# Kernel optimization log

Measured on AMD Instinct MI355X. Metric: run time of the kernel, lower is better.

Reference implementation:

```python
import jax, jax.numpy as jnp
import numpy as np

B, N, D, H = 2, 2048, 1024, 16
DK = D // H


def setup_inputs() -> dict:
    key = jax.random.key(0)
    ks = jax.random.split(key, 12)
    s = D ** -0.5
    inp = {
        "query": jax.random.normal(ks[0], (B, N, D), jnp.float32),
        "key": jax.random.normal(ks[1], (B, N, D), jnp.float32),
        "value": jax.random.normal(ks[2], (B, N, D), jnp.float32),
        # causal mask: 1 = keep, 0 = masked (matches create_causal_mask)
        "mask": jnp.tril(jnp.ones((N, N), jnp.int32)),
        "Wq": jax.random.normal(ks[3], (D, D), jnp.float32) * s,
        "bq": jnp.zeros((D,), jnp.float32),
        "Wk": jax.random.normal(ks[4], (D, D), jnp.float32) * s,
        "bk": jnp.zeros((D,), jnp.float32),
        "Wv": jax.random.normal(ks[5], (D, D), jnp.float32) * s,
        "bv": jnp.zeros((D,), jnp.float32),
        "Wo": jax.random.normal(ks[6], (D, D), jnp.float32) * s,
        "bo": jnp.zeros((D,), jnp.float32),
    }
    return inp


def reference(query, key, value, mask, Wq, bq, Wk, bk, Wv, bv, Wo, bo):
    scale = DK ** -0.5
    # Linear projections (torch nn.Linear: x @ W.T + b), split into heads -> [B,H,N,DK]
    q = (query @ Wq.T + bq).reshape(B, N, H, DK).transpose(0, 2, 1, 3)
    k = (key @ Wk.T + bk).reshape(B, N, H, DK).transpose(0, 2, 1, 3)
    v = (value @ Wv.T + bv).reshape(B, N, H, DK).transpose(0, 2, 1, 3)
    scores = jnp.einsum("bhqd,bhkd->bhqk", q, k) * scale  # [B,H,N,N]
    scores = jnp.where(mask[None, None, :, :] == 0, jnp.float32(-1e9), scores)
    attn = jax.nn.softmax(scores, axis=-1)
    ctx = jnp.einsum("bhqk,bhkd->bhqd", attn, v)  # [B,H,N,DK]
    ctx = ctx.transpose(0, 2, 1, 3).reshape(B, N, D)
    return ctx @ Wo.T + bo
```

## Files before the change

### kernel.cpp

```cpp
#include <hip/hip_runtime.h>
#include <hip/hip_bf16.h>

typedef __attribute__((ext_vector_type(4))) float f32x4;
typedef __attribute__((ext_vector_type(8))) __bf16 bf16x8;
typedef __attribute__((ext_vector_type(8))) unsigned short u16x8;
typedef __attribute__((ext_vector_type(4))) unsigned short u16x4;
typedef __attribute__((ext_vector_type(2))) unsigned int u32x2;
typedef unsigned short u16;

#define DEV static __device__ __forceinline__

DEV u16 f2bf(float f){
  unsigned u = __builtin_bit_cast(unsigned, f);
  u += 0x7fff + ((u >> 16) & 1);
  return (u16)(u >> 16);
}

DEV unsigned cvtpk(float lo, float hi){
  unsigned r;
  asm("v_cvt_pk_bf16_f32 %0, %1, %2" : "=v"(r) : "v"(lo), "v"(hi));
  return r;
}

DEV f32x4 mfma16(bf16x8 a, bf16x8 b, f32x4 c){
  return __builtin_amdgcn_mfma_f32_16x16x32_bf16(a, b, c, 0, 0, 0);
}

DEV void gload16(const void* g, void* l){
  __builtin_amdgcn_global_load_lds((const __attribute__((address_space(1))) void*)g,
                                   (__attribute__((address_space(3))) void*)l,
                                   16, 0, 0);
}

DEV float fexp2(float x){
#if __has_builtin(__builtin_amdgcn_exp2f)
  return __builtin_amdgcn_exp2f(x);
#else
  float r; asm("v_exp_f32 %0, %1" : "=v"(r) : "v"(x)); return r;
#endif
}

#define SCL 0.18033688011f
#define THR 11.0f
#define PLD 72

__global__ __launch_bounds__(256) void cvtW_k(
    const float* __restrict__ s0, const float* __restrict__ s1,
    const float* __restrict__ s2, const float* __restrict__ s3,
    u16* __restrict__ d0, u16* __restrict__ d1,
    u16* __restrict__ d2, u16* __restrict__ d3){
  const int y = blockIdx.y;
  const float* __restrict__ s = y==0?s0:y==1?s1:y==2?s2:s3;
  u16* __restrict__ d         = y==0?d0:y==1?d1:y==2?d2:d3;
  const int i = blockIdx.x*256 + threadIdx.x;
  f32x4 a = *(const f32x4*)&s[(size_t)i*8];
  f32x4 b = *(const f32x4*)&s[(size_t)i*8 + 4];
  u16x8 h;
  #pragma unroll
  for (int j = 0; j < 4; ++j){ h[j] = f2bf(a[j]); h[j+4] = f2bf(b[j]); }
  *(u16x8*)&d[(size_t)i*8] = h;
}

DEV bf16x8 rdH(const u16* Hs, int r, int kc, int lhi, int l7){
  int gr = (kc*4 + lhi) ^ l7;
  return *(const bf16x8*)&Hs[r*64 + gr*8];
}

DEV bf16x8 rdF(const float* Fs, int r, int kc, int lhi, int l15){
  int g0 = kc*8 + lhi*2, g1 = g0 + 1;
  f32x4 a = *(const f32x4*)&Fs[r*64 + ((g0 ^ l15)*4)];
  f32x4 b = *(const f32x4*)&Fs[r*64 + ((g1 ^ l15)*4)];
  union { unsigned u[4]; bf16x8 v; } x;
  x.u[0] = cvtpk(a[0], a[1]);
  x.u[1] = cvtpk(a[2], a[3]);
  x.u[2] = cvtpk(b[0], b[1]);
  x.u[3] = cvtpk(b[2], b[3]);
  return x.v;
}

__global__ __launch_bounds__(256) void gemm_qkv2(
    const float* __restrict__ Xq, const float* __restrict__ Xk, const float* __restrict__ Xv,
    const u16* __restrict__ Wq, const u16* __restrict__ Wk, const u16* __restrict__ Wv,
    const float* __restrict__ Bq, const float* __restrict__ Bk, const float* __restrict__ Bv,
    u16* __restrict__ Oq, u16* __restrict__ Ok, u16* __restrict__ Ov){
  __shared__ float Fs[128*64];
  __shared__ u16  Hs[128*64];

  const int f = blockIdx.x;
  const int xc = f & 7, g = f >> 3;
  const int p  = xc*12 + (g >> 3);
  const int bn8 = g & 7;
  const int z = p >> 5, bm32 = p & 31;
  const bool vt = (z == 2);
  const int bm = vt ? bn8 : bm32;
  const int bn = vt ? bm32 : bn8;

  const float* __restrict__ Xz = z==0 ? Xq : z==1 ? Xk : Xv;
  const u16*  __restrict__ Wz  = z==0 ? Wq : z==1 ? Wk : Wv;
  const float* __restrict__ bias = z==0 ? Bq : z==1 ? Bk : Bv;
  u16* __restrict__ C = z==0 ? Oq : z==1 ? Ok : Ov;
  const float qs = (z==0) ? SCL : 1.0f;

  const int tid = threadIdx.x, lane = tid & 63, w = tid >> 6;
  const int wr = w >> 1, wc = w & 1;
  const int l16 = lane & 15, lhi = lane >> 4, l7 = l16 & 7;

  const int frow = tid >> 4, fcol = ((tid & 15) ^ (frow & 15)) * 4;
  const int hrow = tid >> 3, hcol = ((tid & 7) ^ (hrow & 7)) * 8;
  const int fblk = vt ? bn : bm;
  const int hblk = vt ? bm : bn;
  const float* Fsrc = Xz + (size_t)(fblk*128 + frow)*1024 + fcol;
  const u16*  Hsrc  = Wz + (size_t)(hblk*128 + hrow)*1024 + hcol;

  f32x4 acc[4][4] = {};

  for (int k0 = 0; k0 < 1024; k0 += 64){
    __syncthreads();
    #pragma unroll
    for (int j = 0; j < 8; ++j)
      gload16(Fsrc + k0 + (size_t)j*16*1024, Fs + j*1024 + w*256);
    #pragma unroll
    for (int j = 0; j < 4; ++j)
      gload16(Hsrc + k0 + (size_t)j*32*1024, Hs + j*2048 + w*512);
    __syncthreads();

    #pragma unroll
    for (int kc = 0; kc < 2; ++kc){
      bf16x8 fa[4], fb[4];
      if (!vt){
        #pragma unroll
        for (int mi = 0; mi < 4; ++mi) fa[mi] = rdF(Fs, wr*64 + mi*16 + l16, kc, lhi, l16);
        #pragma unroll
        for (int nf = 0; nf < 4; ++nf) fb[nf] = rdH(Hs, wc*64 + nf*16 + l16, kc, lhi, l7);
      } else {
        #pragma unroll
        for (int mi = 0; mi < 4; ++mi) fa[mi] = rdH(Hs, wr*64 + mi*16 + l16, kc, lhi, l7);
        #pragma unroll
        for (int nf = 0; nf < 4; ++nf) fb[nf] = rdF(Fs, wc*64 + nf*16 + l16, kc, lhi, l16);
      }
      #pragma unroll
      for (int mi = 0; mi < 4; ++mi)
        #pragma unroll
        for (int nf = 0; nf < 4; ++nf)
          acc[mi][nf] = mfma16(fa[mi], fb[nf], acc[mi][nf]);
    }
  }

  #pragma unroll
  for (int mi = 0; mi < 4; ++mi){
    #pragma unroll
    for (int nf = 0; nf < 4; ++nf){
      int row0 = bm*128 + wr*64 + mi*16 + lhi*4;
      int col  = bn*128 + wc*64 + nf*16 + l16;
      float bc = bias[col];
      #pragma unroll
      for (int r = 0; r < 4; ++r){
        int row = row0 + r;
        float val = (acc[mi][nf][r] + (vt ? bias[row] : bc)) * qs;
        if (!vt){
          int b = row >> 11, n = row & 2047;
          int h = col >> 6,  dk = col & 63;
          C[(((size_t)(b*16 + h))*2048 + n)*64 + dk] = f2bf(val);
        } else {
          int h = row >> 6,  dk = row & 63;
          int b = col >> 11, n = col & 2047;
          C[(((size_t)(b*16 + h))*64 + dk)*2048 + n] = f2bf(val);
        }
      }
    }
  }
}

__global__ __launch_bounds__(256) void gemm_o64(const u16* __restrict__ A,
                                                const u16* __restrict__ Bw,
                                                const float* __restrict__ bias,
                                                float* __restrict__ C){
  __shared__ u16 As[64*32];
  __shared__ u16 Bs[128*32];
  const int f = blockIdx.x;
  const int bm = (f & 7)*8 + ((f >> 3) >> 3);
  const int bn = (f >> 3) & 7;
  const int tid  = threadIdx.x;
  const int lane = tid & 63, w = tid >> 6;
  const int wr = w >> 1, wc = w & 1;
  const int l16 = lane & 15, lhi = lane >> 4;

  const int srow = w*16 + (lane >> 2);
  const int scol = (lane & 3)*8;
  const u16* Asrc = A  + (size_t)(bm*64  + srow)*1024 + scol;
  const u16* Bsrc = Bw + (size_t)(bn*128 + srow)*1024 + scol;
  u16* Adst0 = As + w*512;
  u16* Bdst0 = Bs + w*512;

  f32x4 acc[2][4] = {};

  for (int k0 = 0; k0 < 1024; k0 += 32){
    __syncthreads();
    gload16(Asrc + k0,             Adst0);
    gload16(Bsrc + k0,             Bdst0);
    gload16(Bsrc + 64*1024 + k0,   Bdst0 + 2048);
    __syncthreads();

    bf16x8 af[2], bfr[4];
    #pragma unroll
    for (int mi = 0; mi < 2; ++mi)
      af[mi] = *(const bf16x8*)&As[(wr*32 + mi*16 + l16)*32 + lhi*8];
    #pragma unroll
    for (int nf = 0; nf < 4; ++nf)
      bfr[nf] = *(const bf16x8*)&Bs[(wc*64 + nf*16 + l16)*32 + lhi*8];
    #pragma unroll
    for (int mi = 0; mi < 2; ++mi)
      #pragma unroll
      for (int nf = 0; nf < 4; ++nf)
        acc[mi][nf] = mfma16(af[mi], bfr[nf], acc[mi][nf]);
  }

  #pragma unroll
  for (int mi = 0; mi < 2; ++mi){
    #pragma unroll
    for (int nf = 0; nf < 4; ++nf){
      int row0 = bm*64 + wr*32 + mi*16 + lhi*4;
      int col  = bn*128 + wc*64 + nf*16 + l16;
      float bv = bias[col];
      #pragma unroll
      for (int r = 0; r < 4; ++r)
        C[(size_t)(row0 + r)*1024 + col] = acc[mi][nf][r] + bv;
    }
  }
}

DEV void sm_tile(int t, int qt, int q_abs,
                 const u16* __restrict__ Ksb, u16* __restrict__ PsW,
                 bf16x8 bq0, bf16x8 bq1,
                 f32x4* ctx, float& m_r, float& l_r,
                 int l16, int lhi, int lane, int swz){
  f32x4 s4[4] = {};
  #pragma unroll
  for (int nf = 0; nf < 4; ++nf){
    bf16x8 ak0 = *(const bf16x8*)&Ksb[(nf*16 + l16)*64 + ((lhi*8) ^ swz)];
    bf16x8 ak1 = *(const bf16x8*)&Ksb[(nf*16 + l16)*64 + ((32 + lhi*8) ^ swz)];
    s4[nf] = mfma16(ak0, bq0, s4[nf]);
    s4[nf] = mfma16(ak1, bq1, s4[nf]);
  }

  if (t == qt){
    #pragma unroll
    for (int nf = 0; nf < 4; ++nf)
      #pragma unroll
      for (int r = 0; r < 4; ++r){
        int kc = t*64 + nf*16 + lhi*4 + r;
        if (kc > q_abs) s4[nf][r] = -1.0e30f;
      }
  }

  float mt = fmaxf(
      fmaxf(fmaxf(fmaxf(s4[0][0],s4[0][1]), fmaxf(s4[0][2],s4[0][3])),
            fmaxf(fmaxf(s4[1][0],s4[1][1]), fmaxf(s4[1][2],s4[1][3]))),
      fmaxf(fmaxf(fmaxf(s4[2][0],s4[2][1]), fmaxf(s4[2][2],s4[2][3])),
            fmaxf(fmaxf(s4[3][0],s4[3][1]), fmaxf(s4[3][2],s4[3][3]))));
  mt = fmaxf(mt, __shfl_xor(mt, 16));
  mt = fmaxf(mt, __shfl_xor(mt, 32));

  if (!__all(mt <= m_r + THR)){
    float mn = fmaxf(m_r, mt);
    float sf = fexp2(m_r - mn);
    m_r = mn;
    l_r *= sf;
    float sfb[4];
    #pragma unroll
    for (int r = 0; r < 4; ++r)
      sfb[r] = __shfl(sf, (lane >> 4)*4 + r);
    #pragma unroll
    for (int dkf = 0; dkf < 4; ++dkf)
      #pragma unroll
      for (int r = 0; r < 4; ++r)
        ctx[dkf][r] *= sfb[r];
  }

  float lt = 0.f;
  u16* prow = PsW + l16*PLD;
  #pragma unroll
  for (int nf = 0; nf < 4; ++nf){
    float p0 = fexp2(s4[nf][0] - m_r);
    float p1 = fexp2(s4[nf][1] - m_r);
    float p2 = fexp2(s4[nf][2] - m_r);
    float p3 = fexp2(s4[nf][3] - m_r);
    lt += (p0 + p1) + (p2 + p3);
    unsigned w0 = __builtin_amdgcn_perm(__builtin_bit_cast(unsigned, p1),
                                        __builtin_bit_cast(unsigned, p0), 0x07060302u);
    unsigned w1 = __builtin_amdgcn_perm(__builtin_bit_cast(unsigned, p3),
                                        __builtin_bit_cast(unsigned, p2), 0x07060302u);
    u32x2 wp = {w0, w1};
    *(u32x2*)&prow[nf*16 + lhi*4] = wp;
  }
  lt += __shfl_xor(lt, 16);
  lt += __shfl_xor(lt, 32);
  l_r += lt;
}

DEV void pv_tile(const u16* __restrict__ Vsb, const u16* __restrict__ PsW,
                 f32x4* ctx, int l16, int lhi, int swz){
  const u16* prow = PsW + l16*PLD;
  __builtin_amdgcn_s_setprio(1);
  #pragma unroll
  for (int ks = 0; ks < 2; ++ks){
    bf16x8 pa = *(const bf16x8*)&prow[ks*32 + lhi*8];
    #pragma unroll
    for (int dkf = 0; dkf < 4; ++dkf){
      bf16x8 vb = *(const bf16x8*)&Vsb[(dkf*16 + l16)*64 + ((ks*32 + lhi*8) ^ swz)];
      ctx[dkf] = mfma16(pa, vb, ctx[dkf]);
    }
  }
  __builtin_amdgcn_s_setprio(0);
}

__global__ __launch_bounds__(256) void attn_k(const u16* __restrict__ Q,
                                              const u16* __restrict__ K,
                                              const u16* __restrict__ Vt,
                                              u16* __restrict__ CTX){
  __shared__ u16 Ks[2][64*64];
  __shared__ u16 Vs[2][64*64];
  __shared__ u16 Ps[4][2][16*PLD];
  const int tid  = threadIdx.x;
  const int lane = tid & 63, w = tid >> 6;
  const int l16 = lane & 15, lhi = lane >> 4;
  const int f  = blockIdx.x;
  const int bh = f & 31;
  const int qt = 31 - (f >> 5);
  const size_t base = (size_t)bh * 2048 * 64;
  const u16* Qb = Q  + base;
  const u16* Kb = K  + base;
  const u16* Vb = Vt + base;
  const int b = bh >> 4, h = bh & 15;

  const int s0 = tid, s1 = tid + 256;
  const int r0 = s0 >> 3, c0 = ((s0 & 7) ^ (r0 & 7))*8;
  const int r1 = s1 >> 3, c1 = ((s1 & 7) ^ (r1 & 7))*8;
  const u16* Ksrc0 = Kb + r0*64 + c0;
  const u16* Ksrc1 = Kb + r1*64 + c1;
  const u16* Vsrc0 = Vb + (size_t)r0*2048 + c0;
  const u16* Vsrc1 = Vb + (size_t)r1*2048 + c1;
  const int swz = (l16 & 7)*8;

  const int q_abs = qt*64 + w*16 + l16;
  bf16x8 bq0 = *(const bf16x8*)&Qb[(size_t)q_abs*64 + lhi*8];
  bf16x8 bq1 = *(const bf16x8*)&Qb[(size_t)q_abs*64 + 32 + lhi*8];

  f32x4 ctx[4] = {};
  float m_r = -3.0e38f, l_r = 0.f;
  u16* Ps0 = &Ps[w][0][0];
  u16* Ps1 = &Ps[w][1][0];

  gload16(Ksrc0, &Ks[0][s0*8]);  gload16(Ksrc1, &Ks[0][s1*8]);
  gload16(Vsrc0, &Vs[0][s0*8]);  gload16(Vsrc1, &Vs[0][s1*8]);
  __syncthreads();

  const int nt = qt + 1;
  for (int t = 0; t < nt; ++t){
    const int pb = t & 1;
    u16* PsC = pb ? Ps1 : Ps0;
    u16* PsP = pb ? Ps0 : Ps1;
    if (t + 1 < nt){
      gload16(Ksrc0 + (t+1)*4096, &Ks[pb^1][s0*8]);
      gload16(Ksrc1 + (t+1)*4096, &Ks[pb^1][s1*8]);
    }
    sm_tile(t, qt, q_abs, Ks[pb], PsC, bq0, bq1, ctx, m_r, l_r, l16, lhi, lane, swz);
    if (t > 0)
      pv_tile(Vs[pb^1], PsP, ctx, l16, lhi, swz);
    __syncthreads();
    if (t + 1 < nt){
      gload16(Vsrc0 + (size_t)(t+1)*64, &Vs[pb^1][s0*8]);
      gload16(Vsrc1 + (size_t)(t+1)*64, &Vs[pb^1][s1*8]);
    }
  }
  pv_tile(Vs[(nt-1)&1], (nt-1)&1 ? Ps1 : Ps0, ctx, l16, lhi, swz);

  float lf[4];
  #pragma unroll
  for (int r = 0; r < 4; ++r)
    lf[r] = __shfl(l_r, (lane >> 4)*4 + r);
  #pragma unroll
  for (int dkf = 0; dkf < 4; ++dkf)
    #pragma unroll
    for (int r = 0; r < 4; ++r){
      int q = qt*64 + w*16 + lhi*4 + r;
      CTX[((size_t)(b*2048 + q))*1024 + h*64 + dkf*16 + l16] = f2bf(ctx[dkf][r] / lf[r]);
    }
}

extern "C" void kernel_launch(void* const* d_in, const int* in_sizes, int n_in,
                              void* d_out, int out_size, void* d_ws, size_t ws_size,
                              hipStream_t stream){
  const float* q  = (const float*)d_in[0];
  const float* k  = (const float*)d_in[1];
  const float* v  = (const float*)d_in[2];
  const float* Wq = (const float*)d_in[4];  const float* bq = (const float*)d_in[5];
  const float* Wk = (const float*)d_in[6];  const float* bk = (const float*)d_in[7];
  const float* Wv = (const float*)d_in[8];  const float* bv = (const float*)d_in[9];
  const float* Wo = (const float*)d_in[10]; const float* bo = (const float*)d_in[11];
  float* out = (float*)d_out;
  dim3 blk(256);

  u16* Wqb = (u16*)d_ws;
  u16* Wkb = Wqb + 1048576;
  u16* Wvb = Wkb + 1048576;
  u16* Wob = Wvb + 1048576;
  u16* Qw  = Wob + 1048576;
  u16* Kw  = Qw + 4194304;
  u16* Vw  = Kw + 4194304;
  u16* Cw  = Vw + 4194304;

  cvtW_k<<<dim3(512, 4), blk, 0, stream>>>(Wq, Wk, Wv, Wo, Wqb, Wkb, Wvb, Wob);
  gemm_qkv2<<<dim3(768), blk, 0, stream>>>(q, k, v, Wqb, Wkb, Wvb,
                                           bq, bk, bv, Qw, Kw, Vw);
  attn_k<<<dim3(1024), blk, 0, stream>>>(Qw, Kw, Vw, Cw);
  gemm_o64<<<dim3(512), blk, 0, stream>>>(Cw, Wob, bo, out);
}
```

Baseline: 135.3 us.

## Pre-convert activations to bf16 in a separate pass and simplify QKV GEMM

```diff
diff --git a/kernel.cpp b/kernel.cpp
--- a/kernel.cpp
+++ b/kernel.cpp
@@ -16,12 +16,6 @@
   return (u16)(u >> 16);
 }
 
-DEV unsigned cvtpk(float lo, float hi){
-  unsigned r;
-  asm("v_cvt_pk_bf16_f32 %0, %1, %2" : "=v"(r) : "v"(lo), "v"(hi));
-  return r;
-}
-
 DEV f32x4 mfma16(bf16x8 a, bf16x8 b, f32x4 c){
   return __builtin_amdgcn_mfma_f32_16x16x32_bf16(a, b, c, 0, 0, 0);
 }
@@ -44,47 +38,40 @@
 #define THR 11.0f
 #define PLD 72
 
-__global__ __launch_bounds__(256) void cvtW_k(
+__global__ __launch_bounds__(256) void cvt_k(
     const float* __restrict__ s0, const float* __restrict__ s1,
     const float* __restrict__ s2, const float* __restrict__ s3,
-    u16* __restrict__ d0, u16* __restrict__ d1,
-    u16* __restrict__ d2, u16* __restrict__ d3){
+    const float* __restrict__ s4, const float* __restrict__ s5,
+    const float* __restrict__ s6,
+    u16* __restrict__ d0, u16* __restrict__ d1, u16* __restrict__ d2,
+    u16* __restrict__ d3, u16* __restrict__ d4, u16* __restrict__ d5,
+    u16* __restrict__ d6){
   const int y = blockIdx.y;
-  const float* __restrict__ s = y==0?s0:y==1?s1:y==2?s2:s3;
-  u16* __restrict__ d         = y==0?d0:y==1?d1:y==2?d2:d3;
-  const int i = blockIdx.x*256 + threadIdx.x;
-  f32x4 a = *(const f32x4*)&s[(size_t)i*8];
-  f32x4 b = *(const f32x4*)&s[(size_t)i*8 + 4];
-  u16x8 h;
-  #pragma unroll
-  for (int j = 0; j < 4; ++j){ h[j] = f2bf(a[j]); h[j+4] = f2bf(b[j]); }
-  *(u16x8*)&d[(size_t)i*8] = h;
-}
-
-DEV bf16x8 rdH(const u16* Hs, int r, int kc, int lhi, int l7){
-  int gr = (kc*4 + lhi) ^ l7;
-  return *(const bf16x8*)&Hs[r*64 + gr*8];
-}
-
-DEV bf16x8 rdF(const float* Fs, int r, int kc, int lhi, int l15){
-  int g0 = kc*8 + lhi*2, g1 = g0 + 1;
-  f32x4 a = *(const f32x4*)&Fs[r*64 + ((g0 ^ l15)*4)];
-  f32x4 b = *(const f32x4*)&Fs[r*64 + ((g1 ^ l15)*4)];
-  union { unsigned u[4]; bf16x8 v; } x;
-  x.u[0] = cvtpk(a[0], a[1]);
-  x.u[1] = cvtpk(a[2], a[3]);
-  x.u[2] = cvtpk(b[0], b[1]);
-  x.u[3] = cvtpk(b[2], b[3]);
-  return x.v;
-}
-
-__global__ __launch_bounds__(256) void gemm_qkv2(
-    const float* __restrict__ Xq, const float* __restrict__ Xk, const float* __restrict__ Xv,
+  const float* __restrict__ s = y==0?s0:y==1?s1:y==2?s2:y==3?s3:y==4?s4:y==5?s5:s6;
+  u16* __restrict__ d         = y==0?d0:y==1?d1:y==2?d2:y==3?d3:y==4?d4:y==5?d5:d6;
+  const int n8 = (y < 3) ? (4096*1024/8) : (1024*1024/8);
+  for (int i = blockIdx.x*256 + threadIdx.x; i < n8; i += gridDim.x*256){
+    f32x4 a = *(const f32x4*)&s[(size_t)i*8];
+    f32x4 b = *(const f32x4*)&s[(size_t)i*8 + 4];
+    u16x8 h;
+    #pragma unroll
+    for (int j = 0; j < 4; ++j){ h[j] = f2bf(a[j]); h[j+4] = f2bf(b[j]); }
+    *(u16x8*)&d[(size_t)i*8] = h;
+  }
+}
+
+DEV bf16x8 rdS(const u16* T, int r, int kc, int lhi){
+  int gr = (kc*4 + lhi) ^ (r & 7);
+  return *(const bf16x8*)&T[r*64 + gr*8];
+}
+
+__global__ __launch_bounds__(256) void gemm_qkv3(
+    const u16* __restrict__ Xq, const u16* __restrict__ Xk, const u16* __restrict__ Xv,
     const u16* __restrict__ Wq, const u16* __restrict__ Wk, const u16* __restrict__ Wv,
     const float* __restrict__ Bq, const float* __restrict__ Bk, const float* __restrict__ Bv,
     u16* __restrict__ Oq, u16* __restrict__ Ok, u16* __restrict__ Ov){
-  __shared__ float Fs[128*64];
-  __shared__ u16  Hs[128*64];
+  __shared__ u16 As[128*64];
+  __shared__ u16 Bs[128*64];
 
   const int f = blockIdx.x;
   const int xc = f & 7, g = f >> 3;
@@ -95,54 +82,53 @@
   const int bm = vt ? bn8 : bm32;
   const int bn = vt ? bm32 : bn8;
 
-  const float* __restrict__ Xz = z==0 ? Xq : z==1 ? Xk : Xv;
-  const u16*  __restrict__ Wz  = z==0 ? Wq : z==1 ? Wk : Wv;
+  const u16* __restrict__ A    = z==0 ? Xq : z==1 ? Xk : Wv;
+  const u16* __restrict__ Bw   = z==0 ? Wq : z==1 ? Wk : Xv;
   const float* __restrict__ bias = z==0 ? Bq : z==1 ? Bk : Bv;
   u16* __restrict__ C = z==0 ? Oq : z==1 ? Ok : Ov;
   const float qs = (z==0) ? SCL : 1.0f;
 
   const int tid = threadIdx.x, lane = tid & 63, w = tid >> 6;
   const int wr = w >> 1, wc = w & 1;
-  const int l16 = lane & 15, lhi = lane >> 4, l7 = l16 & 7;
-
-  const int frow = tid >> 4, fcol = ((tid & 15) ^ (frow & 15)) * 4;
-  const int hrow = tid >> 3, hcol = ((tid & 7) ^ (hrow & 7)) * 8;
-  const int fblk = vt ? bn : bm;
-  const int hblk = vt ? bm : bn;
-  const float* Fsrc = Xz + (size_t)(fblk*128 + frow)*1024 + fcol;
-  const u16*  Hsrc  = Wz + (size_t)(hblk*128 + hrow)*1024 + hcol;
+  const int l16 = lane & 15, lhi = lane >> 4;
+
+  const u16* Asrc[4];
+  const u16* Bsrc[4];
+  #pragma unroll
+  for (int j = 0; j < 4; ++j){
+    int s = tid + j*256;
+    int row = s >> 3;
+    int col = ((s & 7) ^ (row & 7)) * 8;
+    Asrc[j] = A  + (size_t)(bm*128 + row)*1024 + col;
+    Bsrc[j] = Bw + (size_t)(bn*128 + row)*1024 + col;
+  }
 
   f32x4 acc[4][4] = {};
 
   for (int k0 = 0; k0 < 1024; k0 += 64){
     __syncthreads();
     #pragma unroll
-    for (int j = 0; j < 8; ++j)
-      gload16(Fsrc + k0 + (size_t)j*16*1024, Fs + j*1024 + w*256);
-    #pragma unroll
     for (int j = 0; j < 4; ++j)
-      gload16(Hsrc + k0 + (size_t)j*32*1024, Hs + j*2048 + w*512);
+      gload16(Asrc[j] + k0, As + (tid + j*256)*8);
+    #pragma unroll
+    for (int j = 0; j < 4; ++j)
+      gload16(Bsrc[j] + k0, Bs + (tid + j*256)*8);
     __syncthreads();
 
     #pragma unroll
     for (int kc = 0; kc < 2; ++kc){
-      bf16x8 fa[4], fb[4];
-      if (!vt){
-        #pragma unroll
-        for (int mi = 0; mi < 4; ++mi) fa[mi] = rdF(Fs, wr*64 + mi*16 + l16, kc, lhi, l16);
-        #pragma unroll
-        for (int nf = 0; nf < 4; ++nf) fb[nf] = rdH(Hs, wc*64 + nf*16 + l16, kc, lhi, l7);
-      } else {
-        #pragma unroll
-        for (int mi = 0; mi < 4; ++mi) fa[mi] = rdH(Hs, wr*64 + mi*16 + l16, kc, lhi, l7);
-        #pragma unroll
-        for (int nf = 0; nf < 4; ++nf) fb[nf] = rdF(Fs, wc*64 + nf*16 + l16, kc, lhi, l16);
-      }
+      bf16x8 af[4], bfr[4];
+      #pragma unroll
+      for (int mi = 0; mi < 4; ++mi)
+        af[mi] = rdS(As, wr*64 + mi*16 + l16, kc, lhi);
+      #pragma unroll
+      for (int nf = 0; nf < 4; ++nf)
+        bfr[nf] = rdS(Bs, wc*64 + nf*16 + l16, kc, lhi);
       #pragma unroll
       for (int mi = 0; mi < 4; ++mi)
         #pragma unroll
         for (int nf = 0; nf < 4; ++nf)
-          acc[mi][nf] = mfma16(fa[mi], fb[nf], acc[mi][nf]);
+          acc[mi][nf] = mfma16(af[mi], bfr[nf], acc[mi][nf]);
     }
   }
 
@@ -405,13 +391,17 @@
   u16* Wkb = Wqb + 1048576;
   u16* Wvb = Wkb + 1048576;
   u16* Wob = Wvb + 1048576;
-  u16* Qw  = Wob + 1048576;
+  u16* Xqb = Wob + 1048576;
+  u16* Xkb = Xqb + 4194304;
+  u16* Xvb = Xkb + 4194304;
+  u16* Qw  = Xvb + 4194304;
   u16* Kw  = Qw + 4194304;
   u16* Vw  = Kw + 4194304;
-  u16* Cw  = Vw + 4194304;
-
-  cvtW_k<<<dim3(512, 4), blk, 0, stream>>>(Wq, Wk, Wv, Wo, Wqb, Wkb, Wvb, Wob);
-  gemm_qkv2<<<dim3(768), blk, 0, stream>>>(q, k, v, Wqb, Wkb, Wvb,
+  u16* Cw  = Xqb;
+
+  cvt_k<<<dim3(512, 7), blk, 0, stream>>>(q, k, v, Wq, Wk, Wv, Wo,
+                                          Xqb, Xkb, Xvb, Wqb, Wkb, Wvb, Wob);
+  gemm_qkv3<<<dim3(768), blk, 0, stream>>>(Xqb, Xkb, Xvb, Wqb, Wkb, Wvb,
                                            bq, bk, bv, Qw, Kw, Vw);
   attn_k<<<dim3(1024), blk, 0, stream>>>(Qw, Kw, Vw, Cw);
   gemm_o64<<<dim3(512), blk, 0, stream>>>(Cw, Wob, bo, out);
```

After: 133.1 us. About the same (-1.6%).
